# Kernel optimization log

Hardware: AMD Instinct MI355X
Metric: run time of the kernel (lower is better)

## Reference

```python
import math
import jax, jax.numpy as jnp
import numpy as np

B, T, C, NH = 2, 2048, 2048, 16
HD = C // NH  # 128


def _quantize_int6(key, out_f, in_f):
    """Replicates Int6LinearDynamic.reset_parameters/_quantize_update."""
    w = jax.random.normal(key, (out_f, in_f), jnp.float32) * (1.0 / math.sqrt(in_f))
    max_val = jnp.clip(jnp.max(jnp.abs(w), axis=1, keepdims=True), 1e-5)
    scale = max_val / 31.0
    w_int = jnp.clip(jnp.round(w / scale), -32, 31).astype(jnp.int8)
    return w_int, scale.squeeze(1)  # [out,in] int8, [out] f32


def setup_inputs() -> dict:
    key = jax.random.key(0)
    k_x, k_a, k_p = jax.random.split(key, 3)
    attn_w, attn_scales = _quantize_int6(k_a, 3 * C, C)
    proj_w, proj_scales = _quantize_int6(k_p, C, C)
    return {
        "x": jax.random.normal(k_x, (B, T, C), jnp.float32),
        "attn_w": attn_w,
        "attn_scales": attn_scales,
        "proj_w": proj_w,
        "proj_scales": proj_scales,
        "qk_gain": jnp.float32(1.0),
    }


def _l2norm(t):
    # F.normalize(p=2, dim=-1, eps=1e-12)
    n = jnp.sqrt(jnp.sum(t * t, axis=-1, keepdims=True))
    return t / jnp.maximum(n, 1e-12)


def reference(x, attn_w, attn_scales, proj_w, proj_scales, qk_gain):
    # dequantized int6 GEMM: w = int8 * per-row scale
    wa = attn_w.astype(jnp.float32) * attn_scales[:, None]  # [3C, C]
    qkv = jnp.einsum("btc,oc->bto", x, wa)                   # [B,T,3C]
    q, k, v = jnp.split(qkv, 3, axis=2)

    def heads(t):  # [B,T,C] -> [B,NH,T,HD]
        return t.reshape(B, T, NH, HD).transpose(0, 2, 1, 3)

    q, k, v = heads(q), heads(k), heads(v)
    q = _l2norm(q) * qk_gain
    k = _l2norm(k) * qk_gain

    # causal SDPA, default scale 1/sqrt(head_dim)
    scores = jnp.einsum("bhqd,bhkd->bhqk", q, k) / math.sqrt(HD)
    causal = jnp.tril(jnp.ones((T, T), dtype=bool))
    scores = jnp.where(causal, scores, -jnp.inf)
    attn = jax.nn.softmax(scores, axis=-1)
    y = jnp.einsum("bhqk,bhkd->bhqd", attn, v)               # [B,NH,T,HD]
    y = y.transpose(0, 2, 1, 3).reshape(B, T, C)

    wp = proj_w.astype(jnp.float32) * proj_scales[:, None]   # [C, C]
    return jnp.einsum("btc,oc->bto", y, wp)
```

## Files before the change

kernel.cpp:

```cpp
#include <hip/hip_runtime.h>


#define DEVINL __device__ __forceinline__

typedef unsigned short u16;
typedef __bf16 bf16x8 __attribute__((ext_vector_type(8)));
typedef float  f32x4  __attribute__((ext_vector_type(4)));
typedef float  f32x16 __attribute__((ext_vector_type(16)));
typedef short  short8 __attribute__((ext_vector_type(8)));
typedef u16    u16x4  __attribute__((ext_vector_type(4)));
typedef unsigned uint4x __attribute__((ext_vector_type(4)));

static constexpr int T_  = 2048;
static constexpr int C_  = 2048;
static constexpr int TC3 = 6144;

DEVINL u16 f2bf(float f) {
  union { float f; unsigned u; } v; v.f = f;
  unsigned r = v.u + 0x7FFFu + ((v.u >> 16) & 1u);
  return (u16)(r >> 16);
}
DEVINL float bf2f(u16 s) {
  union { unsigned u; float f; } v; v.u = ((unsigned)s) << 16;
  return v.f;
}
DEVINL bf16x8 ld8(const u16* p) {
  return __builtin_bit_cast(bf16x8, *(const short8*)p);
}
DEVINL f32x4 mfma16(bf16x8 a, bf16x8 b, f32x4 c) {
  return __builtin_amdgcn_mfma_f32_16x16x32_bf16(a, b, c, 0, 0, 0);
}
DEVINL f32x16 mfma32(bf16x8 a, bf16x8 b, f32x16 c) {
  return __builtin_amdgcn_mfma_f32_32x32x16_bf16(a, b, c, 0, 0, 0);
}
DEVINL void async_cp16(const u16* gp, u16* lp) {
  __builtin_amdgcn_global_load_lds(
      (const __attribute__((address_space(1))) void*)gp,
      (__attribute__((address_space(3))) void*)lp, 16, 0, 0);
}
DEVINL unsigned cvtpk(float lo, float hi) {
  unsigned r;
  asm("v_cvt_pk_bf16_f32 %0, %1, %2" : "=v"(r) : "v"(lo), "v"(hi));
  return r;
}
DEVINL void plswap(unsigned& a, unsigned& b) {
  asm("v_permlane32_swap_b32 %0, %1" : "+v"(a), "+v"(b));
}

__global__ __launch_bounds__(256) void k_cast_x(const float* __restrict__ in,
                                                u16* __restrict__ out) {
  long i = (long)(blockIdx.x * 256 + threadIdx.x) * 4;
  float4 v = *(const float4*)(in + i);
  u16x4 o; o.x = f2bf(v.x); o.y = f2bf(v.y); o.z = f2bf(v.z); o.w = f2bf(v.w);
  *(u16x4*)(out + i) = o;
}
__global__ __launch_bounds__(256) void k_cast_w(const int* __restrict__ in,
                                                u16* __restrict__ out) {
  long i = (long)(blockIdx.x * 256 + threadIdx.x) * 4;
  int4 v = *(const int4*)(in + i);
  u16x4 o; o.x = f2bf((float)v.x); o.y = f2bf((float)v.y);
  o.z = f2bf((float)v.z); o.w = f2bf((float)v.w);
  *(u16x4*)(out + i) = o;
}

template<bool OUT_BF16>
__global__ __launch_bounds__(256) void k_gemm_bt(
    const u16* __restrict__ A, const u16* __restrict__ Bt,
    const float* __restrict__ scale, void* __restrict__ Cv,
    int N, long K) {
  __shared__ u16 As[128 * 32];
  __shared__ u16 Bs[128 * 32];
  const int tid  = threadIdx.x;
  const int wave = tid >> 6;
  const int lane = tid & 63;
  const int l15  = lane & 15;
  const int quad = lane >> 4;
  const int wm = (wave & 1) * 64;
  const int wn = (wave >> 1) * 64;
  const long bm = (long)blockIdx.y * 128;
  const long bn = (long)blockIdx.x * 128;

  f32x4 acc[4][4] = {};

  const int srow = lane >> 2;
  const int scol = (lane & 3) * 8;

  for (long k0 = 0; k0 < K; k0 += 32) {
#pragma unroll
    for (int i = 0; i < 2; ++i) {
      const int j = wave * 2 + i;
      const int row = j * 16 + srow;
      async_cp16(A  + (bm + row) * K + k0 + scol, &As[j * 512]);
      async_cp16(Bt + (bn + row) * K + k0 + scol, &Bs[j * 512]);
    }
    __syncthreads();
    bf16x8 af[4], bfr[4];
#pragma unroll
    for (int mi = 0; mi < 4; ++mi)
      af[mi] = ld8(&As[(wm + mi * 16 + l15) * 32 + quad * 8]);
#pragma unroll
    for (int ni = 0; ni < 4; ++ni)
      bfr[ni] = ld8(&Bs[(wn + ni * 16 + l15) * 32 + quad * 8]);
#pragma unroll
    for (int mi = 0; mi < 4; ++mi)
#pragma unroll
      for (int ni = 0; ni < 4; ++ni)
        acc[mi][ni] = mfma16(af[mi], bfr[ni], acc[mi][ni]);
    __syncthreads();
  }
#pragma unroll
  for (int ni = 0; ni < 4; ++ni) {
    const long col = bn + wn + ni * 16 + l15;
    const float sc = scale[col];
#pragma unroll
    for (int mi = 0; mi < 4; ++mi) {
      const long row0 = bm + wm + mi * 16 + quad * 4;
#pragma unroll
      for (int r = 0; r < 4; ++r) {
        float v = acc[mi][ni][r] * sc;
        if constexpr (OUT_BF16) ((u16*)Cv)[(row0 + r) * (long)N + col] = f2bf(v);
        else                    ((float*)Cv)[(row0 + r) * (long)N + col] = v;
      }
    }
  }
}

__global__ __launch_bounds__(256) void k_norm_qk(u16* __restrict__ qkv,
                                                 const float* __restrict__ qk_gain) {
  const int token = blockIdx.x;
  const int wave = threadIdx.x >> 6, lane = threadIdx.x & 63;
  const float g = qk_gain[0];
  const float qmul = g * g * 1.44269504f * 0.08838834764f;
  u16* rowp = qkv + (long)token * TC3;
#pragma unroll
  for (int s = 0; s < 8; ++s) {
    const int seg = wave * 8 + s;
    const int isK = seg >> 4;
    const int h = seg & 15;
    u16* ptr = rowp + isK * C_ + h * 128 + lane * 2;
    unsigned pv = *(const unsigned*)ptr;
    float a = bf2f((u16)(pv & 0xffffu));
    float bb = bf2f((u16)(pv >> 16));
    float ss = a * a + bb * bb;
#pragma unroll
    for (int m = 1; m <= 32; m <<= 1) ss += __shfl_xor(ss, m);
    float denom = fmaxf(sqrtf(ss), 1e-12f);
    float f = (isK ? 1.0f : qmul) / denom;
    u16 o0 = f2bf(a * f), o1 = f2bf(bb * f);
    *(unsigned*)ptr = (unsigned)o0 | ((unsigned)o1 << 16);
  }
}

__global__ __launch_bounds__(256) void k_vt(const u16* __restrict__ qkv,
                                            u16* __restrict__ vt) {
  const int t0 = blockIdx.x * 64;
  const int h = blockIdx.y, bz = blockIdx.z;
  const int t = threadIdx.x & 63;
  const int d0 = threadIdx.x >> 6;
  const long tokbase = (long)bz * T_;
  const u16* src = qkv + (tokbase + t0 + t) * (long)TC3 + 2 * C_ + h * 128;
  u16* dst = vt + ((long)(bz * 16 + h) * 128) * (long)T_ + t0 + t;
#pragma unroll
  for (int dd = 0; dd < 32; ++dd) {
    const int d = dd * 4 + d0;
    dst[(long)d * T_] = src[d];
  }
}

__global__ __launch_bounds__(256, 2) void k_attn(const u16* __restrict__ qkv,
                                                 const u16* __restrict__ vtg,
                                                 u16* __restrict__ y) {
  const int qt = blockIdx.z ? (15 - blockIdx.x) : blockIdx.x;
  const int h  = blockIdx.y;
  const int bz = blockIdx.z;
  const int tid = threadIdx.x, w = tid >> 6, lane = tid & 63;
  const int m31 = lane & 31, hi = lane >> 5;

  __shared__ u16 Ks[2][64 * 128];
  __shared__ u16 Vt[2][128 * 64];

  const long tokbase = (long)bz * T_;
  const int qbase = qt * 128 + w * 32;
  const u16* vbase = vtg + ((long)(bz * 16 + h) * 128) * (long)T_;
  const u16* kbase = qkv + tokbase * TC3 + C_ + h * 128;

  bf16x8 qf[8];
  {
    const u16* qp = qkv + (tokbase + qbase + m31) * (long)TC3 + h * 128 + hi * 8;
#pragma unroll
    for (int kc = 0; kc < 8; ++kc)
      qf[kc] = ld8(qp + kc * 16);
  }

  f32x16 o[4];
#pragma unroll
  for (int i = 0; i < 4; ++i)
#pragma unroll
    for (int r = 0; r < 16; ++r) o[i][r] = 0.f;
  f32x4 lacc = {0.f, 0.f, 0.f, 0.f};

  auto stage = [&](int ktb, int b) {
#pragma unroll
    for (int j = 0; j < 4; ++j) {
      const int t = w * 4 + j;
      const int p = t * 64 + lane;
      const int r  = p >> 4, ck = p & 15;
      async_cp16(kbase + (long)(ktb + r) * TC3 + ((ck ^ (r & 15)) * 8),
                 &Ks[b][t * 512]);
      const int d  = p >> 3, cv = p & 7;
      async_cp16(vbase + (long)d * T_ + ktb + ((cv ^ (d & 7)) * 8),
                 &Vt[b][t * 512]);
    }
  };

  stage(0, 0);
  __syncthreads();
  int b = 0;
  const int ktmax = 2 * qt + 1;

  for (int kt = 0; kt <= ktmax; ++kt) {
    const int ktb = kt * 64;
    if (kt < ktmax) stage(ktb + 64, b ^ 1);

    if (ktb <= qbase + 31) {
      f32x16 sA[2];
      __builtin_amdgcn_s_setprio(1);
#pragma unroll
      for (int kb = 0; kb < 2; ++kb) {
        f32x16 acc;
#pragma unroll
        for (int r = 0; r < 16; ++r) acc[r] = 0.f;
#pragma unroll
        for (int kc = 0; kc < 8; ++kc) {
          bf16x8 kf = ld8(&Ks[b][(kb * 32 + m31) * 128 +
                                 (((2 * kc + hi) ^ (lane & 15)) * 8)]);
          acc = mfma32(kf, qf[kc], acc);
        }
        sA[kb] = acc;
      }
      __builtin_amdgcn_s_setprio(0);

      if (ktb + 63 > qbase) {
        const int qq = qbase + m31;
#pragma unroll
        for (int kb = 0; kb < 2; ++kb)
#pragma unroll
          for (int r = 0; r < 16; ++r) {
            const int key = ktb + kb * 32 + (r & 3) + 8 * (r >> 2) + 4 * hi;
            if (key > qq) sA[kb][r] = -1e30f;
          }
      }
#pragma unroll
      for (int kb = 0; kb < 2; ++kb)
#pragma unroll
        for (int r = 0; r < 16; ++r) {
          float p = __builtin_amdgcn_exp2f(sA[kb][r]);
          sA[kb][r] = p;
          lacc[r & 3] += p;
        }

      bf16x8 pb[4];
#pragma unroll
      for (int ks = 0; ks < 4; ++ks) {
        const int kb = ks >> 1, j = ks & 1;
        unsigned w0a = cvtpk(sA[kb][8 * j + 0], sA[kb][8 * j + 1]);
        unsigned w1a = cvtpk(sA[kb][8 * j + 2], sA[kb][8 * j + 3]);
        unsigned w0b = cvtpk(sA[kb][8 * j + 4], sA[kb][8 * j + 5]);
        unsigned w1b = cvtpk(sA[kb][8 * j + 6], sA[kb][8 * j + 7]);
        plswap(w0a, w0b);
        plswap(w1a, w1b);
        uint4x t; t.x = w0a; t.y = w1a; t.z = w0b; t.w = w1b;
        pb[ks] = __builtin_bit_cast(bf16x8, t);
      }

      __builtin_amdgcn_s_setprio(1);
#pragma unroll
      for (int db = 0; db < 4; ++db)
#pragma unroll
        for (int ks = 0; ks < 4; ++ks) {
          bf16x8 vf = ld8(&Vt[b][(db * 32 + m31) * 64 +
                                 (((2 * ks + hi) ^ (m31 & 7)) * 8)]);
          o[db] = mfma32(vf, pb[ks], o[db]);
        }
      __builtin_amdgcn_s_setprio(0);
    }

    if (kt < ktmax) __syncthreads();
    b ^= 1;
  }

  float lrow = lacc[0] + lacc[1] + lacc[2] + lacc[3];
  lrow += __shfl_xor(lrow, 32);
  const float inv_l = 1.0f / lrow;
  u16* yp = y + (tokbase + qbase + m31) * (long)C_ + h * 128 + 4 * hi;
#pragma unroll
  for (int db = 0; db < 4; ++db)
#pragma unroll
    for (int g = 0; g < 4; ++g) {
      u16x4 pk;
#pragma unroll
      for (int r = 0; r < 4; ++r) pk[r] = f2bf(o[db][g * 4 + r] * inv_l);
      *(u16x4*)(yp + db * 32 + g * 8) = pk;
    }
}

extern "C" void kernel_launch(void* const* d_in, const int* in_sizes, int n_in,
                              void* d_out, int out_size, void* d_ws, size_t ws_size,
                              hipStream_t stream) {
  const float* x    = (const float*)d_in[0];
  const int*   aw   = (const int*)d_in[1];
  const float* asc  = (const float*)d_in[2];
  const int*   pw   = (const int*)d_in[3];
  const float* psc  = (const float*)d_in[4];
  const float* gain = (const float*)d_in[5];

  char* ws = (char*)d_ws;
  u16* xb  = (u16*)(ws);
  u16* wab = (u16*)(ws + 16777216UL);
  u16* wpb = (u16*)(ws + 41943040UL);
  u16* qkv = (u16*)(ws + 50331648UL);
  u16* yb  = (u16*)(ws + 100663296UL);
  u16* vtg = xb;

  k_cast_x<<<8192, 256, 0, stream>>>(x, xb);
  k_cast_w<<<12288, 256, 0, stream>>>(aw, wab);
  k_cast_w<<<4096, 256, 0, stream>>>(pw, wpb);
  k_gemm_bt<true><<<dim3(48, 32), 256, 0, stream>>>(xb, wab, asc, qkv, TC3, (long)C_);
  k_norm_qk<<<4096, 256, 0, stream>>>(qkv, gain);
  k_vt<<<dim3(32, 16, 2), 256, 0, stream>>>(qkv, vtg);
  k_attn<<<dim3(16, 16, 2), 256, 0, stream>>>(qkv, vtg, yb);
  k_gemm_bt<false><<<dim3(16, 32), 256, 0, stream>>>(yb, wpb, psc, (float*)d_out, C_, (long)C_);
}
```

Measured before the change: 421.0 us.

## Replace QKV GEMM with 256x256-tile, 8-wave pipelined kernel

Adds a new GEMM kernel for the QKV projection that uses 256x256 output tiles with 512 threads and double-buffered LDS. Global-to-LDS async copies are issued in quarter-tiles interleaved with MFMA phases, with explicit vmcnt waits, barriers and setprio. The larger tiles raise data reuse per block, and the interleaving is meant to hide load latency behind compute. The grid shrinks to 384 blocks and LDS use rises to 128 KB per block, which may limit occupancy and leave CUs unevenly loaded in the final wave.

Result: no change. 428.5 us (+1.8%).

```diff
diff --git a/kernel.cpp b/kernel.cpp
--- a/kernel.cpp
+++ b/kernel.cpp
@@ -45,6 +45,13 @@
 }
 DEVINL void plswap(unsigned& a, unsigned& b) {
   asm("v_permlane32_swap_b32 %0, %1" : "+v"(a), "+v"(b));
+}
+template<int N> DEVINL void vmwait() {
+  if constexpr (N == 0)       asm volatile("s_waitcnt vmcnt(0)" ::: "memory");
+  else if constexpr (N == 2)  asm volatile("s_waitcnt vmcnt(2)" ::: "memory");
+  else if constexpr (N == 6)  asm volatile("s_waitcnt vmcnt(6)" ::: "memory");
+  else if constexpr (N == 8)  asm volatile("s_waitcnt vmcnt(8)" ::: "memory");
+  else if constexpr (N == 10) asm volatile("s_waitcnt vmcnt(10)" ::: "memory");
 }
 
 __global__ __launch_bounds__(256) void k_cast_x(const float* __restrict__ in,
@@ -125,6 +132,159 @@
   }
 }
 
+DEVINL void stage_q(const u16* __restrict__ G, long brow, long K, int tt, int qi,
+                    u16 (&L)[2][256 * 64], int w, int lane) {
+  const int sr = w * 8 + (lane >> 3);
+  const int sc = lane & 7;
+  const long grow = brow + qi * 64 + sr;
+  async_cp16(G + grow * K + (long)(tt << 6) + ((sc ^ (sr & 7)) << 3),
+             &L[tt & 1][(qi * 64 + w * 8) * 64]);
+}
+
+template<int WP1, int WP3, bool ISS0, bool ISS123, bool LAST>
+DEVINL void kstep256(int t, const u16* __restrict__ A, const u16* __restrict__ Bt,
+                     long K, long bm, long bn,
+                     u16 (&As)[2][256 * 64], u16 (&Bs)[2][256 * 64],
+                     f32x4 (&acc)[8][4], int w, int lane) {
+  const int l15 = lane & 15, quad = lane >> 4;
+  const int wm = (w & 1) * 128;
+  const int wn = (w >> 1) * 64;
+  const int buf = t & 1;
+
+  auto rdA = [&](int mi, int kc) -> bf16x8 {
+    const int row = wm + mi * 16 + l15;
+    const int k0 = kc * 32 + quad * 8;
+    return ld8(&As[buf][row * 64 + (k0 ^ ((row & 7) * 8))]);
+  };
+  auto rdB = [&](int ni, int kc) -> bf16x8 {
+    const int row = wn + ni * 16 + l15;
+    const int k0 = kc * 32 + quad * 8;
+    return ld8(&Bs[buf][row * 64 + (k0 ^ ((row & 7) * 8))]);
+  };
+
+  bf16x8 af[4][2], bfl[2][2];
+#pragma unroll
+  for (int mi = 0; mi < 4; ++mi) { af[mi][0] = rdA(mi, 0); af[mi][1] = rdA(mi, 1); }
+#pragma unroll
+  for (int ni = 0; ni < 2; ++ni) { bfl[ni][0] = rdB(ni, 0); bfl[ni][1] = rdB(ni, 1); }
+  if constexpr (ISS0) {
+    stage_q(A, bm, K, t + 1, 1, As, w, lane);
+    stage_q(A, bm, K, t + 1, 3, As, w, lane);
+  }
+  __builtin_amdgcn_s_barrier();
+  __builtin_amdgcn_s_setprio(1);
+#pragma unroll
+  for (int mi = 0; mi < 4; ++mi)
+#pragma unroll
+    for (int ni = 0; ni < 2; ++ni) {
+      acc[mi][ni] = mfma16(af[mi][0], bfl[ni][0], acc[mi][ni]);
+      acc[mi][ni] = mfma16(af[mi][1], bfl[ni][1], acc[mi][ni]);
+    }
+  __builtin_amdgcn_s_setprio(0);
+  __builtin_amdgcn_s_barrier();
+
+  bf16x8 bfh[2][2];
+#pragma unroll
+  for (int ni = 0; ni < 2; ++ni) { bfh[ni][0] = rdB(2 + ni, 0); bfh[ni][1] = rdB(2 + ni, 1); }
+  if constexpr (ISS123) {
+    stage_q(A, bm, K, t + 2, 0, As, w, lane);
+    stage_q(A, bm, K, t + 2, 2, As, w, lane);
+  }
+  __builtin_amdgcn_s_barrier();
+  __builtin_amdgcn_s_setprio(1);
+#pragma unroll
+  for (int mi = 0; mi < 4; ++mi)
+#pragma unroll
+    for (int ni = 0; ni < 2; ++ni) {
+      acc[mi][2 + ni] = mfma16(af[mi][0], bfh[ni][0], acc[mi][2 + ni]);
+      acc[mi][2 + ni] = mfma16(af[mi][1], bfh[ni][1], acc[mi][2 + ni]);
+    }
+  __builtin_amdgcn_s_setprio(0);
+  vmwait<WP1>();
+  __builtin_amdgcn_s_barrier();
+
+  bf16x8 af2[4][2];
+#pragma unroll
+  for (int mi = 0; mi < 4; ++mi) { af2[mi][0] = rdA(4 + mi, 0); af2[mi][1] = rdA(4 + mi, 1); }
+  if constexpr (ISS123) {
+    stage_q(Bt, bn, K, t + 2, 0, Bs, w, lane);
+    stage_q(Bt, bn, K, t + 2, 1, Bs, w, lane);
+  }
+  __builtin_amdgcn_s_barrier();
+  __builtin_amdgcn_s_setprio(1);
+#pragma unroll
+  for (int mi = 0; mi < 4; ++mi)
+#pragma unroll
+    for (int ni = 0; ni < 2; ++ni) {
+      acc[4 + mi][2 + ni] = mfma16(af2[mi][0], bfh[ni][0], acc[4 + mi][2 + ni]);
+      acc[4 + mi][2 + ni] = mfma16(af2[mi][1], bfh[ni][1], acc[4 + mi][2 + ni]);
+    }
+  __builtin_amdgcn_s_setprio(0);
+  __builtin_amdgcn_s_barrier();
+
+  if constexpr (ISS123) {
+    stage_q(Bt, bn, K, t + 2, 2, Bs, w, lane);
+    stage_q(Bt, bn, K, t + 2, 3, Bs, w, lane);
+  }
+  __builtin_amdgcn_s_setprio(1);
+#pragma unroll
+  for (int mi = 0; mi < 4; ++mi)
+#pragma unroll
+    for (int ni = 0; ni < 2; ++ni) {
+      acc[4 + mi][ni] = mfma16(af2[mi][0], bfl[ni][0], acc[4 + mi][ni]);
+      acc[4 + mi][ni] = mfma16(af2[mi][1], bfl[ni][1], acc[4 + mi][ni]);
+    }
+  __builtin_amdgcn_s_setprio(0);
+  if constexpr (!LAST) {
+    vmwait<WP3>();
+    __builtin_amdgcn_s_barrier();
+  }
+}
+
+__global__ __launch_bounds__(512, 2) void k_gemm256(
+    const u16* __restrict__ A, const u16* __restrict__ Bt,
+    const float* __restrict__ scale, u16* __restrict__ C,
+    int N, long K) {
+  __shared__ u16 As[2][256 * 64];
+  __shared__ u16 Bs[2][256 * 64];
+  const int tid = threadIdx.x, w = tid >> 6, lane = tid & 63;
+  const long bm = (long)blockIdx.y * 256;
+  const long bn = (long)blockIdx.x * 256;
+  const int nt = (int)(K >> 6);
+
+  stage_q(A, bm, K, 0, 0, As, w, lane); stage_q(A, bm, K, 0, 2, As, w, lane);
+  stage_q(Bt, bn, K, 0, 0, Bs, w, lane); stage_q(Bt, bn, K, 0, 1, Bs, w, lane);
+  stage_q(Bt, bn, K, 0, 2, Bs, w, lane); stage_q(Bt, bn, K, 0, 3, Bs, w, lane);
+  stage_q(A, bm, K, 0, 1, As, w, lane); stage_q(A, bm, K, 0, 3, As, w, lane);
+  stage_q(A, bm, K, 1, 0, As, w, lane); stage_q(A, bm, K, 1, 2, As, w, lane);
+  stage_q(Bt, bn, K, 1, 0, Bs, w, lane); stage_q(Bt, bn, K, 1, 1, Bs, w, lane);
+  stage_q(Bt, bn, K, 1, 2, Bs, w, lane); stage_q(Bt, bn, K, 1, 3, Bs, w, lane);
+  vmwait<6>();
+  __builtin_amdgcn_s_barrier();
+
+  f32x4 acc[8][4] = {};
+  int t = 0;
+  for (; t < nt - 2; ++t)
+    kstep256<10, 8, true, true, false>(t, A, Bt, K, bm, bn, As, Bs, acc, w, lane);
+  kstep256<8, 2, true, false, false>(nt - 2, A, Bt, K, bm, bn, As, Bs, acc, w, lane);
+  kstep256<0, 0, false, false, true>(nt - 1, A, Bt, K, bm, bn, As, Bs, acc, w, lane);
+
+  const int l15 = lane & 15, quad = lane >> 4;
+  const int wm = (w & 1) * 128, wn = (w >> 1) * 64;
+#pragma unroll
+  for (int ni = 0; ni < 4; ++ni) {
+    const long col = bn + wn + ni * 16 + l15;
+    const float sc = scale[col];
+#pragma unroll
+    for (int mi = 0; mi < 8; ++mi) {
+      const long row0 = bm + wm + mi * 16 + quad * 4;
+#pragma unroll
+      for (int r = 0; r < 4; ++r)
+        C[(row0 + r) * (long)N + col] = f2bf(acc[mi][ni][r] * sc);
+    }
+  }
+}
+
 __global__ __launch_bounds__(256) void k_norm_qk(u16* __restrict__ qkv,
                                                  const float* __restrict__ qk_gain) {
   const int token = blockIdx.x;
@@ -325,7 +485,7 @@
   k_cast_x<<<8192, 256, 0, stream>>>(x, xb);
   k_cast_w<<<12288, 256, 0, stream>>>(aw, wab);
   k_cast_w<<<4096, 256, 0, stream>>>(pw, wpb);
-  k_gemm_bt<true><<<dim3(48, 32), 256, 0, stream>>>(xb, wab, asc, qkv, TC3, (long)C_);
+  k_gemm256<<<dim3(24, 16), 512, 0, stream>>>(xb, wab, asc, qkv, TC3, (long)C_);
   k_norm_qk<<<4096, 256, 0, stream>>>(qkv, gain);
   k_vt<<<dim3(32, 16, 2), 256, 0, stream>>>(qkv, vtg);
   k_attn<<<dim3(16, 16, 2), 256, 0, stream>>>(qkv, vtg, yb);
```
